# Kernel optimization log

Measured on AMD Instinct MI355X. Metric: run time of the kernel, lower is better.

## Reference

```python
import jax, jax.numpy as jnp
import numpy as np

NUM_HEADS = 16

def setup_inputs() -> dict:
    key = jax.random.key(0)
    k1, k2, k3 = jax.random.split(key, 3)
    B, N, C = 2, 2048, 1024
    x = jax.random.normal(k1, (B, N, C), dtype=jnp.float32)
    Wqkv = jax.random.normal(k2, (3 * C, C), dtype=jnp.float32) * (C ** -0.5)
    Wproj = jax.random.normal(k3, (C, C), dtype=jnp.float32) * (C ** -0.5)
    bproj = jnp.zeros((C,), dtype=jnp.float32)
    return {"x": x, "Wqkv": Wqkv, "Wproj": Wproj, "bproj": bproj}

def reference(x, Wqkv, Wproj, bproj):
    B, N, C = x.shape
    H = NUM_HEADS
    D = C // H
    scale = D ** -0.5
    # torch Linear: y = x @ W^T ; qkv -> [B,N,3,H,D]
    qkv = (x @ Wqkv.T).reshape(B, N, 3, H, D)
    q = qkv[:, :, 0].transpose(0, 2, 1, 3)  # [B,H,N,D]
    k = qkv[:, :, 1].transpose(0, 2, 1, 3)
    v = qkv[:, :, 2].transpose(0, 2, 1, 3)
    attn = jnp.einsum('bhnd,bhmd->bhnm', q, k) * scale  # [B,H,N,N]
    attn = jax.nn.softmax(attn, axis=-1)
    out = jnp.einsum('bhnm,bhmd->bhnd', attn, v)  # [B,H,N,D]
    out = out.transpose(0, 2, 1, 3).reshape(B, N, C)
    return out @ Wproj.T + bproj
```

## Files before the change

kernel.cpp:

```cpp
#include <hip/hip_runtime.h>

typedef unsigned short u16;
typedef unsigned int u32;
typedef __attribute__((ext_vector_type(8))) short short8;
typedef __attribute__((ext_vector_type(8))) __bf16 bf16x8;
typedef __attribute__((ext_vector_type(4))) float f32x4;
typedef __attribute__((ext_vector_type(16))) float f32x16;
typedef __attribute__((ext_vector_type(4))) unsigned short us4;
typedef __attribute__((ext_vector_type(4))) unsigned int u32x4;

#define DEVFN static __device__ __forceinline__

DEVFN u16 f2bf(float f) {
  u32 u = __float_as_uint(f);
  return (u16)((u + 0x7fffu + ((u >> 16) & 1u)) >> 16);
}

#if __has_builtin(__builtin_amdgcn_exp2f)
DEVFN float fexp2(float x) { return __builtin_amdgcn_exp2f(x); }
#else
DEVFN float fexp2(float x) { return exp2f(x); }
#endif

template <typename T>
DEVFN auto mfma16_imp(T a, T b, f32x4 c, int)
    -> decltype(__builtin_amdgcn_mfma_f32_16x16x32_bf16(a, b, c, 0, 0, 0)) {
  return __builtin_amdgcn_mfma_f32_16x16x32_bf16(a, b, c, 0, 0, 0);
}
template <typename T>
DEVFN f32x4 mfma16_imp(T a, T b, f32x4 c, long) {
  return __builtin_amdgcn_mfma_f32_16x16x32_bf16(
      __builtin_bit_cast(bf16x8, a), __builtin_bit_cast(bf16x8, b), c, 0, 0, 0);
}
DEVFN f32x4 MFMA(short8 a, short8 b, f32x4 c) { return mfma16_imp(a, b, c, 0); }

template <typename T>
DEVFN auto mfma32_imp(T a, T b, f32x16 c, int)
    -> decltype(__builtin_amdgcn_mfma_f32_32x32x16_bf16(a, b, c, 0, 0, 0)) {
  return __builtin_amdgcn_mfma_f32_32x32x16_bf16(a, b, c, 0, 0, 0);
}
template <typename T>
DEVFN f32x16 mfma32_imp(T a, T b, f32x16 c, long) {
  return __builtin_amdgcn_mfma_f32_32x32x16_bf16(
      __builtin_bit_cast(bf16x8, a), __builtin_bit_cast(bf16x8, b), c, 0, 0, 0);
}
DEVFN f32x16 MFMA32(short8 a, short8 b, f32x16 c) { return mfma32_imp(a, b, c, 0); }

DEVFN void gload_lds16(const u16* g, u16* l) {
  __builtin_amdgcn_global_load_lds(
      (__attribute__((address_space(1))) void*)g,
      (__attribute__((address_space(3))) void*)l, 16, 0, 0);
}

DEVFN u32 cvtpk_bf16(float lo, float hi) {
  u32 w;
  asm("v_cvt_pk_bf16_f32 %0, %1, %2" : "=v"(w) : "v"(lo), "v"(hi));
  return w;
}

__global__ void __launch_bounds__(256) cvt_all(
    const float* __restrict__ x, u16* __restrict__ xo,
    const float* __restrict__ w1, u16* __restrict__ w1o,
    const float* __restrict__ w2, u16* __restrict__ w2o) {
  int bid = blockIdx.x;
  const float* in;
  u16* out;
  int i;
  if (bid < 4096) {
    in = x; out = xo; i = bid * 256 + threadIdx.x;
  } else if (bid < 7168) {
    in = w1; out = w1o; i = (bid - 4096) * 256 + threadIdx.x;
  } else {
    in = w2; out = w2o; i = (bid - 7168) * 256 + threadIdx.x;
  }
  f32x4 v = ((const f32x4*)in)[i];
  us4 o;
  o[0] = f2bf(v[0]); o[1] = f2bf(v[1]); o[2] = f2bf(v[2]); o[3] = f2bf(v[3]);
  ((us4*)out)[i] = o;
}

template <int F32OUT>
DEVFN void gemm_tile(const u16* __restrict__ A, const u16* __restrict__ Bm,
                     u16* __restrict__ Cbf, float* __restrict__ Cf,
                     const float* __restrict__ bias, int N, int K, int bm,
                     int bn, u16* As, u16* Bs) {
  const int tid = threadIdx.x;
  const int wave = tid >> 6, lane = tid & 63;
  const int wr = (wave >> 1) * 64, wc = (wave & 1) * 64;
  const int srow = lane >> 2, scol = (lane & 3) * 8;
  const int fr = lane & 15, fk = (lane >> 4) * 8;

  f32x4 acc[4][4] = {};

  for (int k0 = 0; k0 < K; k0 += 32) {
    __syncthreads();
#pragma unroll
    for (int t = 0; t < 2; ++t) {
      int rr = (wave * 2 + t) * 16 + srow;
      gload_lds16(A + (size_t)(bm + rr) * K + k0 + scol, As + (wave * 2 + t) * 512);
      gload_lds16(Bm + (size_t)(bn + rr) * K + k0 + scol, Bs + (wave * 2 + t) * 512);
    }
    __syncthreads();
    short8 af[4], bf[4];
#pragma unroll
    for (int i = 0; i < 4; ++i) {
      af[i] = *(const short8*)(As + (wr + i * 16 + fr) * 32 + fk);
      bf[i] = *(const short8*)(Bs + (wc + i * 16 + fr) * 32 + fk);
    }
#pragma unroll
    for (int mi = 0; mi < 4; ++mi)
#pragma unroll
      for (int ni = 0; ni < 4; ++ni)
        acc[mi][ni] = MFMA(af[mi], bf[ni], acc[mi][ni]);
  }

  const int orow = (lane >> 4) * 4, ocol = lane & 15;
#pragma unroll
  for (int mi = 0; mi < 4; ++mi)
#pragma unroll
    for (int ni = 0; ni < 4; ++ni)
#pragma unroll
      for (int r = 0; r < 4; ++r) {
        size_t row = (size_t)(bm + wr + mi * 16 + orow + r);
        size_t col = (size_t)(bn + wc + ni * 16 + ocol);
        if (F32OUT)
          Cf[row * N + col] = acc[mi][ni][r] + bias[col];
        else
          Cbf[row * N + col] = f2bf(acc[mi][ni][r]);
      }
}

template <int F32OUT>
__global__ void __launch_bounds__(256) gemm_bt(
    const u16* __restrict__ A, const u16* __restrict__ Bm,
    u16* __restrict__ Cbf, float* __restrict__ Cf, const float* __restrict__ bias,
    int M, int N, int K) {
  __shared__ u16 As[128 * 32];
  __shared__ u16 Bs[128 * 32];
  gemm_tile<F32OUT>(A, Bm, Cbf, Cf, bias, N, K, blockIdx.x * 128,
                    blockIdx.y * 128, As, Bs);
}

__global__ void __launch_bounds__(256) fused_qkv_gemm(
    const u16* __restrict__ x, const u16* __restrict__ wqkv,
    u16* __restrict__ qk, u16* __restrict__ vt) {
  __shared__ u16 As[128 * 32];
  __shared__ u16 Bs[128 * 32];
  int bid = blockIdx.x;
  if (bid < 512) {
    gemm_tile<0>(x, wqkv, qk, nullptr, nullptr, 2048, 1024, (bid & 31) * 128,
                 (bid >> 5) * 128, As, Bs);
  } else {
    int j = bid - 512;
    gemm_tile<0>(wqkv + (size_t)2048 * 1024, x, vt, nullptr, nullptr, 4096,
                 1024, (j & 7) * 128, (j >> 3) * 128, As, Bs);
  }
}

__global__ void __launch_bounds__(256) attn_kernel(const u16* __restrict__ qk,
                                                   const u16* __restrict__ vT,
                                                   u16* __restrict__ attn_out) {
  __shared__ u16 Ks[2][64 * 64];
  __shared__ u16 Vs[2][64 * 64];

  const int tid = threadIdx.x;
  const int wave = tid >> 6, lane = tid & 63;
  const int q5 = lane & 31, hi = lane >> 5;
  const int qb = blockIdx.x, h = blockIdx.y, b = blockIdx.z;
  const size_t tok0 = (size_t)b * 2048;
  const float SCALE = 0.18033688011112042f;

  const size_t qrow = tok0 + qb * 128 + wave * 32 + q5;
  const u16* qp = qk + qrow * 2048 + h * 64 + hi * 8;
  short8 qf[4];
#pragma unroll
  for (int ks = 0; ks < 4; ++ks) qf[ks] = *(const short8*)(qp + ks * 16);

  const u16* kbase = qk + tok0 * 2048 + 1024 + h * 64;
  const u16* vtb = vT + (size_t)h * 64 * 4096 + tok0;

  const int rowl = lane >> 3;
  const int k_srcoff = ((lane & 7) ^ rowl) * 8;

  float m_run = -1e30f, l_run = 0.f;
  f32x16 o0 = {}, o1 = {};

#define STAGE(kv0, buf)                                                        \
  {                                                                            \
    _Pragma("unroll") for (int c = 0; c < 2; ++c) {                            \
      int rw = c * 4 + wave;                                                   \
      int row = rw * 8 + rowl;                                                 \
      gload_lds16(kbase + (size_t)((kv0) + row) * 2048 + k_srcoff,             \
                  Ks[buf] + rw * 512);                                         \
      int vso = (((lane & 7) ^ rowl ^ rw) * 8);    \
      gload_lds16(vtb + (size_t)row * 4096 + (kv0) + vso, Vs[buf] + rw * 512); \
    }                                                                          \
  }

  STAGE(0, 0);
  __syncthreads();

  for (int t = 0; t < 32; ++t) {
    const int cur = t & 1, nxt = cur ^ 1;
    if (t < 31) STAGE((t + 1) * 64, nxt);

    const u16* Kc = Ks[cur];
    f32x16 s0 = {}, s1 = {};
    __builtin_amdgcn_s_setprio(1);
#pragma unroll
    for (int ks = 0; ks < 4; ++ks) {
      int ch = ((ks * 2 + hi) ^ (q5 & 7)) * 8;
      short8 k0 = *(const short8*)(Kc + q5 * 64 + ch);
      short8 k1 = *(const short8*)(Kc + (32 + q5) * 64 + ch);
      s0 = MFMA32(k0, qf[ks], s0);
      s1 = MFMA32(k1, qf[ks], s1);
    }
    __builtin_amdgcn_s_setprio(0);

    float mt[8];
#pragma unroll
    for (int i = 0; i < 8; ++i)
      mt[i] = fmaxf(fmaxf(s0[i], s0[i + 8]), fmaxf(s1[i], s1[i + 8]));
    float pmax = fmaxf(fmaxf(fmaxf(mt[0], mt[1]), fmaxf(mt[2], mt[3])),
                       fmaxf(fmaxf(mt[4], mt[5]), fmaxf(mt[6], mt[7])));
    pmax = fmaxf(pmax, __shfl_xor(pmax, 32, 64));
    float mraw = pmax * SCALE;

    if (__any(mraw > m_run + 8.f)) {
      float mn = fmaxf(m_run, mraw);
      float alpha = fexp2(m_run - mn);
#pragma unroll
      for (int i = 0; i < 16; ++i) { o0[i] *= alpha; o1[i] *= alpha; }
      l_run *= alpha;
      m_run = mn;
    }

    float p0[16], p1[16];
    float rs = 0.f;
#pragma unroll
    for (int i = 0; i < 16; ++i) {
      p0[i] = fexp2(fmaf(s0[i], SCALE, -m_run));
      p1[i] = fexp2(fmaf(s1[i], SCALE, -m_run));
      rs += p0[i] + p1[i];
    }
    rs += __shfl_xor(rs, 32, 64);
    l_run += rs;

    u32 w0[4][2], w1[4][2];
#pragma unroll
    for (int a = 0; a < 4; ++a) {
      w0[a][0] = cvtpk_bf16(p0[4 * a], p0[4 * a + 1]);
      w0[a][1] = cvtpk_bf16(p0[4 * a + 2], p0[4 * a + 3]);
      w1[a][0] = cvtpk_bf16(p1[4 * a], p1[4 * a + 1]);
      w1[a][1] = cvtpk_bf16(p1[4 * a + 2], p1[4 * a + 3]);
    }
    short8 pb[4];
#pragma unroll
    for (int ks = 0; ks < 4; ++ks) {
      int e = ks & 1;
      u32 x0 = (ks < 2) ? w0[2 * e][0] : w1[2 * e][0];
      u32 y0 = (ks < 2) ? w0[2 * e + 1][0] : w1[2 * e + 1][0];
      u32 x1 = (ks < 2) ? w0[2 * e][1] : w1[2 * e][1];
      u32 y1 = (ks < 2) ? w0[2 * e + 1][1] : w1[2 * e + 1][1];
      asm("v_permlane32_swap_b32 %0, %1" : "+v"(x0), "+v"(y0));
      asm("v_permlane32_swap_b32 %0, %1" : "+v"(x1), "+v"(y1));
      u32x4 tt = {x0, x1, y0, y1};
      pb[ks] = __builtin_bit_cast(short8, tt);
    }

    const u16* Vc = Vs[cur];
    __builtin_amdgcn_s_setprio(1);
#pragma unroll
    for (int ks = 0; ks < 4; ++ks) {
      int ch0 = ((ks * 2 + hi) ^ (q5 & 7) ^ ((q5 >> 3) & 7)) * 8;
      int ch1 = ch0 ^ (4 * 8);
      short8 v0 = *(const short8*)(Vc + q5 * 64 + ch0);
      short8 v1 = *(const short8*)(Vc + (32 + q5) * 64 + ch1);
      o0 = MFMA32(v0, pb[ks], o0);
      o1 = MFMA32(v1, pb[ks], o1);
    }
    __builtin_amdgcn_s_setprio(0);

    __syncthreads();
  }
#undef STAGE

  float inv = 1.f / l_run;
#pragma unroll
  for (int dt = 0; dt < 2; ++dt)
#pragma unroll
    for (int g = 0; g < 4; ++g) {
      us4 st;
#pragma unroll
      for (int c2 = 0; c2 < 4; ++c2) {
        float val = (dt == 0 ? o0[4 * g + c2] : o1[4 * g + c2]) * inv;
        st[c2] = f2bf(val);
      }
      int col = h * 64 + dt * 32 + 8 * g + 4 * hi;
      *(us4*)(attn_out + qrow * 1024 + col) = st;
    }
}

extern "C" void kernel_launch(void* const* d_in, const int* in_sizes, int n_in,
                              void* d_out, int out_size, void* d_ws, size_t ws_size,
                              hipStream_t stream) {
  const float* x = (const float*)d_in[0];
  const float* Wqkv = (const float*)d_in[1];
  const float* Wproj = (const float*)d_in[2];
  const float* bproj = (const float*)d_in[3];
  float* out = (float*)d_out;

  char* ws = (char*)d_ws;
  u16* x_bf     = (u16*)(ws);
  u16* wqkv_bf  = (u16*)(ws + 8388608);
  u16* wproj_bf = (u16*)(ws + 14680064);
  u16* qk_bf    = (u16*)(ws + 16777216);
  u16* vt_bf    = (u16*)(ws + 33554432);
  u16* attn_bf  = (u16*)(ws + 41943040);

  cvt_all<<<8192, 256, 0, stream>>>(x, x_bf, Wqkv, wqkv_bf, Wproj, wproj_bf);

  fused_qkv_gemm<<<768, 256, 0, stream>>>(x_bf, wqkv_bf, qk_bf, vt_bf);

  dim3 g2(16, 16, 2);
  attn_kernel<<<g2, 256, 0, stream>>>(qk_bf, vt_bf, attn_bf);

  dim3 g3(32, 8);
  gemm_bt<1><<<g3, 256, 0, stream>>>(attn_bf, wproj_bf, nullptr, out, bproj,
                                     4096, 1024, 1024);
}
```

Measured before the change: 131.0 us.

## Split attention KV range across two wave groups per block and merge softmax states

```diff
diff --git a/kernel.cpp b/kernel.cpp
--- a/kernel.cpp
+++ b/kernel.cpp
@@ -157,20 +157,24 @@
   }
 }
 
-__global__ void __launch_bounds__(256) attn_kernel(const u16* __restrict__ qk,
+__global__ void __launch_bounds__(512) attn_kernel(const u16* __restrict__ qk,
                                                    const u16* __restrict__ vT,
                                                    u16* __restrict__ attn_out) {
-  __shared__ u16 Ks[2][64 * 64];
-  __shared__ u16 Vs[2][64 * 64];
+  __shared__ u16 SM[32768];
 
   const int tid = threadIdx.x;
   const int wave = tid >> 6, lane = tid & 63;
+  const int g = wave >> 2, gw = wave & 3;
   const int q5 = lane & 31, hi = lane >> 5;
   const int qb = blockIdx.x, h = blockIdx.y, b = blockIdx.z;
   const size_t tok0 = (size_t)b * 2048;
   const float SCALE = 0.18033688011112042f;
 
-  const size_t qrow = tok0 + qb * 128 + wave * 32 + q5;
+  u16* const Kg = SM + g * 2 * 4096;
+  u16* const Vg = SM + 16384 + g * 2 * 4096;
+  const int kvoff = g * 1024;
+
+  const size_t qrow = tok0 + qb * 128 + gw * 32 + q5;
   const u16* qp = qk + qrow * 2048 + h * 64 + hi * 8;
   short8 qf[4];
 #pragma unroll
@@ -188,23 +192,24 @@
 #define STAGE(kv0, buf)                                                        \
   {                                                                            \
     _Pragma("unroll") for (int c = 0; c < 2; ++c) {                            \
-      int rw = c * 4 + wave;                                                   \
+      int rw = c * 4 + gw;                                                     \
       int row = rw * 8 + rowl;                                                 \
       gload_lds16(kbase + (size_t)((kv0) + row) * 2048 + k_srcoff,             \
-                  Ks[buf] + rw * 512);                                         \
+                  Kg + (buf) * 4096 + rw * 512);                               \
       int vso = (((lane & 7) ^ rowl ^ rw) * 8);    \
-      gload_lds16(vtb + (size_t)row * 4096 + (kv0) + vso, Vs[buf] + rw * 512); \
+      gload_lds16(vtb + (size_t)row * 4096 + (kv0) + vso,                      \
+                  Vg + (buf) * 4096 + rw * 512);                               \
     }                                                                          \
   }
 
-  STAGE(0, 0);
+  STAGE(kvoff, 0);
   __syncthreads();
 
-  for (int t = 0; t < 32; ++t) {
+  for (int t = 0; t < 16; ++t) {
     const int cur = t & 1, nxt = cur ^ 1;
-    if (t < 31) STAGE((t + 1) * 64, nxt);
-
-    const u16* Kc = Ks[cur];
+    if (t < 15) STAGE(kvoff + (t + 1) * 64, nxt);
+
+    const u16* Kc = Kg + cur * 4096;
     f32x16 s0 = {}, s1 = {};
     __builtin_amdgcn_s_setprio(1);
 #pragma unroll
@@ -268,7 +273,7 @@
       pb[ks] = __builtin_bit_cast(short8, tt);
     }
 
-    const u16* Vc = Vs[cur];
+    const u16* Vc = Vg + cur * 4096;
     __builtin_amdgcn_s_setprio(1);
 #pragma unroll
     for (int ks = 0; ks < 4; ++ks) {
@@ -285,20 +290,39 @@
   }
 #undef STAGE
 
-  float inv = 1.f / l_run;
-#pragma unroll
-  for (int dt = 0; dt < 2; ++dt)
-#pragma unroll
-    for (int g = 0; g < 4; ++g) {
-      us4 st;
-#pragma unroll
-      for (int c2 = 0; c2 < 4; ++c2) {
-        float val = (dt == 0 ? o0[4 * g + c2] : o1[4 * g + c2]) * inv;
-        st[c2] = f2bf(val);
+  float* sm = (float*)SM;
+  float* base = sm + gw * 2176;
+  if (g == 1) {
+    base[lane] = m_run;
+    base[64 + lane] = l_run;
+#pragma unroll
+    for (int i = 0; i < 16; ++i) {
+      base[128 + i * 64 + lane] = o0[i];
+      base[128 + (16 + i) * 64 + lane] = o1[i];
+    }
+  }
+  __syncthreads();
+  if (g == 0) {
+    float m1 = base[lane], l1 = base[64 + lane];
+    float M = fmaxf(m_run, m1);
+    float wa = fexp2(m_run - M), wb = fexp2(m1 - M);
+    float inv = 1.f / (wa * l_run + wb * l1);
+#pragma unroll
+    for (int dt = 0; dt < 2; ++dt)
+#pragma unroll
+      for (int gq = 0; gq < 4; ++gq) {
+        us4 st;
+#pragma unroll
+        for (int c2 = 0; c2 < 4; ++c2) {
+          int i = 4 * gq + c2;
+          float mine = (dt == 0) ? o0[i] : o1[i];
+          float oth = base[128 + (dt * 16 + i) * 64 + lane];
+          st[c2] = f2bf((wa * mine + wb * oth) * inv);
+        }
+        int col = h * 64 + dt * 32 + 8 * gq + 4 * hi;
+        *(us4*)(attn_out + qrow * 1024 + col) = st;
       }
-      int col = h * 64 + dt * 32 + 8 * g + 4 * hi;
-      *(us4*)(attn_out + qrow * 1024 + col) = st;
-    }
+  }
 }
 
 extern "C" void kernel_launch(void* const* d_in, const int* in_sizes, int n_in,
@@ -323,7 +347,7 @@
   fused_qkv_gemm<<<768, 256, 0, stream>>>(x_bf, wqkv_bf, qk_bf, vt_bf);
 
   dim3 g2(16, 16, 2);
-  attn_kernel<<<g2, 256, 0, stream>>>(qk_bf, vt_bf, attn_bf);
+  attn_kernel<<<g2, 512, 0, stream>>>(qk_bf, vt_bf, attn_bf);
 
   dim3 g3(32, 8);
   gemm_bt<1><<<g3, 256, 0, stream>>>(attn_bf, wproj_bf, nullptr, out, bproj,
```

After: 125.3 us. 1.05x faster.
